# Optimization experiments

Hardware: AMD Instinct MI355X
Metric: run time of the kernel (lower is better)

## Reference

```python
import jax, jax.numpy as jnp
import numpy as np
import math

D_MODEL = 1024
NUM_HEADS = 16
D_HEAD = D_MODEL // NUM_HEADS  # 64
B, S = 2, 1024


def setup_inputs() -> dict:
    key = jax.random.key(0)
    ks = jax.random.split(key, 11)
    s = 1.0 / math.sqrt(D_MODEL)
    inp = {
        "Q": jax.random.normal(ks[0], (B, S, D_MODEL), jnp.float32),
        "K": jax.random.normal(ks[1], (B, S, D_MODEL), jnp.float32),
        "V": jax.random.normal(ks[2], (B, S, D_MODEL), jnp.float32),
        "Wq": jax.random.normal(ks[3], (D_MODEL, D_MODEL), jnp.float32) * s,
        "bq": jnp.zeros((D_MODEL,), jnp.float32),
        "Wk": jax.random.normal(ks[4], (D_MODEL, D_MODEL), jnp.float32) * s,
        "bk": jnp.zeros((D_MODEL,), jnp.float32),
        "Wv": jax.random.normal(ks[5], (D_MODEL, D_MODEL), jnp.float32) * s,
        "bv": jnp.zeros((D_MODEL,), jnp.float32),
        "Wo": jax.random.normal(ks[6], (D_MODEL, D_MODEL), jnp.float32) * s,
        "bo": jnp.zeros((D_MODEL,), jnp.float32),
    }
    return inp


def _linear(x, W, b):
    # torch nn.Linear: x @ W.T + b
    return jnp.einsum("bsd,ed->bse", x, W) + b


def _split_heads(x):
    # Faithful to original: view(b, s, d_head, num_heads).transpose(1, 2)
    # -> 'heads' axis has size d_head, per-head dim is num_heads.
    b, s, _ = x.shape
    return x.reshape(b, s, D_HEAD, NUM_HEADS).transpose(0, 2, 1, 3)  # [b, d_head, s, num_heads]


def reference(Q, K, V, Wq, bq, Wk, bk, Wv, bv, Wo, bo):
    q = _split_heads(_linear(Q, Wq, bq))  # [b, h=d_head, s, e=num_heads]
    k = _split_heads(_linear(K, Wk, bk))
    v = _split_heads(_linear(V, Wv, bv))
    scale = 1.0 / math.sqrt(D_MODEL)  # original scales by sqrt(d_model)
    scores = jnp.einsum("bhqe,bhke->bhqk", q, k) * scale
    attn = jax.nn.softmax(scores, axis=-1)
    ctx = jnp.einsum("bhqk,bhke->bhqe", attn, v)  # [b, d_head, s, num_heads]
    # combine_heads: transpose(1,2) then flatten last two dims
    b, h, s, e = ctx.shape
    merged = ctx.transpose(0, 2, 1, 3).reshape(b, s, h * e)
    return _linear(merged, Wo, bo)
```

## Files before the change

kernel.cpp:

```cpp
#include <hip/hip_runtime.h>
#include <cstdint>
#include <cstddef>
#include <math.h>

typedef _Float16 f16;
typedef _Float16 f16x8 __attribute__((ext_vector_type(8)));
typedef _Float16 f16x4 __attribute__((ext_vector_type(4)));
typedef float f32x4 __attribute__((ext_vector_type(4)));
typedef float f32x16 __attribute__((ext_vector_type(16)));

#define MFMA16(A, B, C) __builtin_amdgcn_mfma_f32_16x16x32_f16((A), (B), (C), 0, 0, 0)
#define MFMA32(A, B, C) __builtin_amdgcn_mfma_f32_32x32x16_f16((A), (B), (C), 0, 0, 0)

#if __has_builtin(__builtin_amdgcn_exp2f)
#define EXP2(x) __builtin_amdgcn_exp2f(x)
#else
#define EXP2(x) exp2f(x)
#endif

__device__ __forceinline__ f16x8 ld8(const f16* p) { return *(const f16x8*)p; }
__device__ __forceinline__ void st8(f16* p, f16x8 v) { *(f16x8*)p = v; }
__device__ __forceinline__ void st4(f16* p, f16x4 v) { *(f16x4*)p = v; }

__device__ __forceinline__ void gll16(const f16* g, f16* l) {
    __builtin_amdgcn_global_load_lds(
        (__attribute__((address_space(1))) void*)(uintptr_t)g,
        (__attribute__((address_space(3))) void*)(unsigned)(uintptr_t)l,
        16, 0, 0);
}

__global__ __launch_bounds__(256) void cast_all(
    const float* __restrict__ Q, const float* __restrict__ K, const float* __restrict__ V,
    const float* __restrict__ Wq, const float* __restrict__ Wk, const float* __restrict__ Wv,
    const float* __restrict__ Wo, f16* __restrict__ dst)
{
    size_t e = ((size_t)blockIdx.x * 256 + threadIdx.x) * 8;
    const float* s; size_t r;
    if (e < 2097152)      { s = Q;  r = e; }
    else if (e < 4194304) { s = K;  r = e - 2097152; }
    else if (e < 6291456) { s = V;  r = e - 4194304; }
    else if (e < 7340032) { s = Wq; r = e - 6291456; }
    else if (e < 8388608) { s = Wk; r = e - 7340032; }
    else if (e < 9437184) { s = Wv; r = e - 8388608; }
    else                  { s = Wo; r = e - 9437184; }
    float4 a = *(const float4*)(s + r);
    float4 b = *(const float4*)(s + r + 4);
    f16x8 o;
    o[0]=(f16)a.x; o[1]=(f16)a.y; o[2]=(f16)a.z; o[3]=(f16)a.w;
    o[4]=(f16)b.x; o[5]=(f16)b.y; o[6]=(f16)b.z; o[7]=(f16)b.w;
    st8(dst + e, o);
}

__global__ __launch_bounds__(256) void qkv_gemm(
    const f16* __restrict__ ws, const float* __restrict__ bq,
    const float* __restrict__ bk, const float* __restrict__ bv,
    f16* __restrict__ outbase)
{
    const int bx = blockIdx.x, bm = blockIdx.y;
    const int mat = bx >> 3, bn = bx & 7;
    const f16* A  = ws + (size_t)mat * 2097152;
    const f16* Bw = ws + 6291456 + (size_t)mat * 1048576;
    const float* bias = (mat == 0) ? bq : (mat == 1) ? bk : bv;
    f16* C = outbase + (size_t)mat * 2097152;

    __shared__ f16 As[2 * 4096];
    __shared__ f16 Bs[2 * 8192];
    const int t = threadIdx.x;
    const int w = t >> 6, lane = t & 63, l5 = lane & 31, hh = lane >> 5;
    const int swz = ((lane & 7) ^ (lane >> 3)) * 8;
    const int l7 = l5 & 7;

    const f16* Ap = A  + (size_t)(bm * 64  + w * 8 + (lane >> 3)) * 1024 + swz;
    const f16* Bp = Bw + (size_t)(bn * 128 + w * 8 + (lane >> 3)) * 1024 + swz;

    f32x16 acc[2] = {};

    gll16(Ap,         &As[w * 512]);
    gll16(Ap + 32768, &As[2048 + w * 512]);
    #pragma unroll
    for (int q = 0; q < 4; ++q)
        gll16(Bp + q * 32768, &Bs[q * 2048 + w * 512]);

    #pragma unroll 2
    for (int kt = 0; kt < 16; ++kt) {
        const int cur = kt & 1;
        __syncthreads();
        if (kt < 15) {
            const f16* Ak = Ap + (kt + 1) * 64;
            const f16* Bk = Bp + (kt + 1) * 64;
            f16* Ad = &As[(cur ^ 1) * 4096 + w * 512];
            f16* Bd = &Bs[(cur ^ 1) * 8192 + w * 512];
            gll16(Ak,         Ad);
            gll16(Ak + 32768, Ad + 2048);
            #pragma unroll
            for (int q = 0; q < 4; ++q)
                gll16(Bk + q * 32768, Bd + q * 2048);
        }
        const f16* Ac = &As[cur * 4096];
        const f16* Bc = &Bs[cur * 8192];
        #pragma unroll
        for (int ks = 0; ks < 4; ++ks) {
            const int c = ks * 2 + hh;
            f16x8 bfr = ld8(&Bc[(w * 32 + l5) * 64 + ((c ^ l7) * 8)]);
            f16x8 af0 = ld8(&Ac[ l5       * 64 + ((c ^ l7) * 8)]);
            f16x8 af1 = ld8(&Ac[(32 + l5) * 64 + ((c ^ l7) * 8)]);
            acc[0] = MFMA32(af0, bfr, acc[0]);
            acc[1] = MFMA32(af1, bfr, acc[1]);
        }
    }

    const float qscale = 0.04508422002778009f;
    const int n = bn * 128 + w * 32 + l5;
    const float bv_ = bias[n];
    if (mat == 0) {
        #pragma unroll
        for (int i = 0; i < 2; ++i)
            #pragma unroll
            for (int r = 0; r < 16; ++r) {
                const int m = bm * 64 + i * 32 + (r & 3) + 8 * (r >> 2) + 4 * hh;
                C[(size_t)m * 1024 + n] = (f16)((acc[i][r] + bv_) * qscale);
            }
    } else if (mat == 1) {
        #pragma unroll
        for (int i = 0; i < 2; ++i)
            #pragma unroll
            for (int r = 0; r < 16; ++r) {
                const int m = bm * 64 + i * 32 + (r & 3) + 8 * (r >> 2) + 4 * hh;
                C[(size_t)m * 1024 + n] = (f16)(acc[i][r] + bv_);
            }
    } else {
        const int hN = n >> 4, eN = n & 15;
        #pragma unroll
        for (int i = 0; i < 2; ++i)
            #pragma unroll
            for (int g = 0; g < 4; ++g) {
                const int m0 = bm * 64 + i * 32 + 8 * g + 4 * hh;
                const int bb = m0 >> 10, s0 = m0 & 1023;
                f16x4 pv;
                pv[0] = (f16)(acc[i][4 * g + 0] + bv_);
                pv[1] = (f16)(acc[i][4 * g + 1] + bv_);
                pv[2] = (f16)(acc[i][4 * g + 2] + bv_);
                pv[3] = (f16)(acc[i][4 * g + 3] + bv_);
                st4(C + ((size_t)((bb * 64 + hN) * 16 + eN)) * 1024 + s0, pv);
            }
    }
}

__global__ __launch_bounds__(256, 4) void attn(
    const f16* __restrict__ qlin, const f16* __restrict__ klin,
    const f16* __restrict__ vT, f16* __restrict__ merged)
{
    __shared__ f16 Ks[2][2048];
    __shared__ f16 Vs[2][2176];
    __shared__ f16 Ps[4][1280];

    const int t = threadIdx.x;
    const int w = t >> 6, lane = t & 63;
    const int l5 = lane & 31, hh = lane >> 5, lg = (lane >> 4) & 3, ll = lane & 15;
    const int h = blockIdx.x, qt = blockIdx.y, b = blockIdx.z;

    const int rowQ0 = b * 1024 + qt * 128;
    const int colh = h * 16;

    f16x8 qf = ld8(qlin + (size_t)(rowQ0 + w * 32 + l5) * 1024 + colh + hh * 8);

    const int sp = ((lane & 7) - (lane >> 3)) & 7;
    const f16* kptr = klin + (size_t)(b * 1024 + w * 32 + (lane >> 3) * 4 + (sp >> 1)) * 1024
                      + colh + (sp & 1) * 8;
    const int ve = t >> 4, vk = (t & 15) * 8;
    const f16* vptr = vT + (size_t)((b * 64 + h) * 16 + ve) * 1024 + vk;
    f16* vdst0 = &Vs[0][ve * 136 + vk];
    f16* vdst1 = &Vs[1][ve * 136 + vk];

    int offKa[4];
    #pragma unroll
    for (int mt = 0; mt < 4; ++mt) {
        const int r = mt * 32 + l5, g = r >> 2;
        offKa[mt] = g * 64 + (((((r & 3) * 2 + hh) + g) & 7) * 8);
    }

    float lsum = 0.f;
    f32x4 O0 = {}, O1 = {};
    f16* Pw = Ps[w];

    f16x8 vv = ld8(vptr);
    gll16(kptr, &Ks[0][w * 512]);
    st8(vdst0, vv);

    for (int kt = 0; kt < 8; ++kt) {
        const int cur = kt & 1;
        if (kt < 7) vv = ld8(vptr + (kt + 1) * 128);
        __syncthreads();
        if (kt < 7) {
            gll16(kptr + (size_t)(kt + 1) * 131072, &Ks[cur ^ 1][w * 512]);
            st8(cur ? vdst0 : vdst1, vv);
        }

        #pragma unroll
        for (int mt = 0; mt < 4; ++mt) {
            f16x8 ka = ld8(&Ks[cur][offKa[mt]]);
            f32x16 Sz = {};
            f32x16 S = MFMA32(ka, qf, Sz);

            #pragma unroll
            for (int g = 0; g < 4; ++g) {
                float p0 = EXP2(S[4 * g + 0]);
                float p1 = EXP2(S[4 * g + 1]);
                float p2 = EXP2(S[4 * g + 2]);
                float p3 = EXP2(S[4 * g + 3]);
                lsum += (p0 + p1) + (p2 + p3);
                f16x4 pk;
                pk[0] = (f16)p0; pk[1] = (f16)p1; pk[2] = (f16)p2; pk[3] = (f16)p3;
                st4(&Pw[l5 * 40 + g * 8 + hh * 4], pk);
            }

            f16x8 va  = ld8(&Vs[cur][ll * 136 + mt * 32 + lg * 8]);
            f16x8 pb0 = ld8(&Pw[ll * 40 + lg * 8]);
            f16x8 pb1 = ld8(&Pw[(16 + ll) * 40 + lg * 8]);
            O0 = MFMA16(va, pb0, O0);
            O1 = MFMA16(va, pb1, O1);
        }
    }

    lsum += __shfl_xor(lsum, 32);
    const float i0 = 1.f / __shfl(lsum, ll);
    const float i1 = 1.f / __shfl(lsum, 16 + ll);

    f16x4 o0, o1;
    o0[0]=(f16)(O0[0]*i0); o0[1]=(f16)(O0[1]*i0); o0[2]=(f16)(O0[2]*i0); o0[3]=(f16)(O0[3]*i0);
    o1[0]=(f16)(O1[0]*i1); o1[1]=(f16)(O1[1]*i1); o1[2]=(f16)(O1[2]*i1); o1[3]=(f16)(O1[3]*i1);
    const size_t q0 = rowQ0 + w * 32 + ll;
    st4(merged + q0 * 1024 + colh + lg * 4, o0);
    st4(merged + (q0 + 16) * 1024 + colh + lg * 4, o1);
}

__global__ __launch_bounds__(256) void o_gemm(
    const f16* __restrict__ A, const f16* __restrict__ Bw,
    const float* __restrict__ bias, float* __restrict__ Cf)
{
    const int bn = blockIdx.x, bm = blockIdx.y;
    __shared__ f16 As[2 * 4096];
    __shared__ f16 Bs[2 * 4096];
    const int t = threadIdx.x;
    const int w = t >> 6, lane = t & 63, l5 = lane & 31, hh = lane >> 5;
    const int wr = w >> 1, wc = w & 1;
    const int swz = ((lane & 7) ^ (lane >> 3)) * 8;
    const int l7 = l5 & 7;

    const f16* Ap = A  + (size_t)(bm * 64 + w * 8 + (lane >> 3)) * 1024 + swz;
    const f16* Bp = Bw + (size_t)(bn * 64 + w * 8 + (lane >> 3)) * 1024 + swz;

    f32x16 acc = {};

    gll16(Ap,         &As[w * 512]);
    gll16(Ap + 32768, &As[2048 + w * 512]);
    gll16(Bp,         &Bs[w * 512]);
    gll16(Bp + 32768, &Bs[2048 + w * 512]);

    #pragma unroll 2
    for (int kt = 0; kt < 16; ++kt) {
        const int cur = kt & 1;
        __syncthreads();
        if (kt < 15) {
            const f16* Ak = Ap + (kt + 1) * 64;
            const f16* Bk = Bp + (kt + 1) * 64;
            f16* Ad = &As[(cur ^ 1) * 4096 + w * 512];
            f16* Bd = &Bs[(cur ^ 1) * 4096 + w * 512];
            gll16(Ak,         Ad);
            gll16(Ak + 32768, Ad + 2048);
            gll16(Bk,         Bd);
            gll16(Bk + 32768, Bd + 2048);
        }
        const f16* Ac = &As[cur * 4096];
        const f16* Bc = &Bs[cur * 4096];
        #pragma unroll
        for (int ks = 0; ks < 4; ++ks) {
            const int c = ks * 2 + hh;
            f16x8 af = ld8(&Ac[(wr * 32 + l5) * 64 + ((c ^ l7) * 8)]);
            f16x8 bf = ld8(&Bc[(wc * 32 + l5) * 64 + ((c ^ l7) * 8)]);
            acc = MFMA32(af, bf, acc);
        }
    }

    const int n = bn * 64 + wc * 32 + l5;
    const float bv_ = bias[n];
    #pragma unroll
    for (int r = 0; r < 16; ++r) {
        const int m = bm * 64 + wr * 32 + (r & 3) + 8 * (r >> 2) + 4 * hh;
        Cf[(size_t)m * 1024 + n] = acc[r] + bv_;
    }
}

extern "C" void kernel_launch(void* const* d_in, const int* in_sizes, int n_in,
                              void* d_out, int out_size, void* d_ws, size_t ws_size,
                              hipStream_t stream) {
    (void)in_sizes; (void)n_in; (void)out_size; (void)ws_size;
    const float* Q  = (const float*)d_in[0];
    const float* K  = (const float*)d_in[1];
    const float* V  = (const float*)d_in[2];
    const float* Wq = (const float*)d_in[3];
    const float* bq = (const float*)d_in[4];
    const float* Wk = (const float*)d_in[5];
    const float* bk = (const float*)d_in[6];
    const float* Wv = (const float*)d_in[7];
    const float* bv = (const float*)d_in[8];
    const float* Wo = (const float*)d_in[9];
    const float* bo = (const float*)d_in[10];
    float* out = (float*)d_out;

    f16* ws = (f16*)d_ws;
    f16* qlin   = ws + 10485760;
    f16* klin   = ws + 12582912;
    f16* vT     = ws + 14680064;
    f16* merged = ws + 16777216;
    f16* Woc    = ws + 9437184;

    cast_all<<<5120, 256, 0, stream>>>(Q, K, V, Wq, Wk, Wv, Wo, ws);
    qkv_gemm<<<dim3(24, 32), 256, 0, stream>>>(ws, bq, bk, bv, qlin);
    attn<<<dim3(64, 8, 2), 256, 0, stream>>>(qlin, klin, vT, merged);
    o_gemm<<<dim3(16, 32), 256, 0, stream>>>(merged, Woc, bo, out);
}
```

Before: 160.2 us.

## Enlarge QKV GEMM block tile to 128x128 with 2x2 warp grid

```diff
diff --git a/kernel.cpp b/kernel.cpp
--- a/kernel.cpp
+++ b/kernel.cpp
@@ -51,7 +51,7 @@
     st8(dst + e, o);
 }
 
-__global__ __launch_bounds__(256) void qkv_gemm(
+__global__ __launch_bounds__(256, 2) void qkv_gemm(
     const f16* __restrict__ ws, const float* __restrict__ bq,
     const float* __restrict__ bk, const float* __restrict__ bv,
     f16* __restrict__ outbase)
@@ -63,86 +63,90 @@
     const float* bias = (mat == 0) ? bq : (mat == 1) ? bk : bv;
     f16* C = outbase + (size_t)mat * 2097152;
 
-    __shared__ f16 As[2 * 4096];
-    __shared__ f16 Bs[2 * 8192];
+    __shared__ f16 As[2][8192];
+    __shared__ f16 Bs[2][8192];
     const int t = threadIdx.x;
     const int w = t >> 6, lane = t & 63, l5 = lane & 31, hh = lane >> 5;
+    const int wr = w >> 1, wc = w & 1;
     const int swz = ((lane & 7) ^ (lane >> 3)) * 8;
     const int l7 = l5 & 7;
 
-    const f16* Ap = A  + (size_t)(bm * 64  + w * 8 + (lane >> 3)) * 1024 + swz;
-    const f16* Bp = Bw + (size_t)(bn * 128 + w * 8 + (lane >> 3)) * 1024 + swz;
-
-    f32x16 acc[2] = {};
-
-    gll16(Ap,         &As[w * 512]);
-    gll16(Ap + 32768, &As[2048 + w * 512]);
+    const f16* Ap = A  + (size_t)(bm * 128 + w * 32 + (lane >> 3)) * 1024 + swz;
+    const f16* Bp = Bw + (size_t)(bn * 128 + w * 32 + (lane >> 3)) * 1024 + swz;
+
+    f32x16 acc[2][2] = {};
+
     #pragma unroll
-    for (int q = 0; q < 4; ++q)
-        gll16(Bp + q * 32768, &Bs[q * 2048 + w * 512]);
-
-    #pragma unroll 2
+    for (int q = 0; q < 4; ++q) {
+        gll16(Ap + q * 8192, &As[0][(w * 32 + q * 8) * 64]);
+        gll16(Bp + q * 8192, &Bs[0][(w * 32 + q * 8) * 64]);
+    }
+
     for (int kt = 0; kt < 16; ++kt) {
         const int cur = kt & 1;
         __syncthreads();
         if (kt < 15) {
             const f16* Ak = Ap + (kt + 1) * 64;
             const f16* Bk = Bp + (kt + 1) * 64;
-            f16* Ad = &As[(cur ^ 1) * 4096 + w * 512];
-            f16* Bd = &Bs[(cur ^ 1) * 8192 + w * 512];
-            gll16(Ak,         Ad);
-            gll16(Ak + 32768, Ad + 2048);
-            #pragma unroll
-            for (int q = 0; q < 4; ++q)
-                gll16(Bk + q * 32768, Bd + q * 2048);
-        }
-        const f16* Ac = &As[cur * 4096];
-        const f16* Bc = &Bs[cur * 8192];
+            #pragma unroll
+            for (int q = 0; q < 4; ++q) {
+                gll16(Ak + q * 8192, &As[cur ^ 1][(w * 32 + q * 8) * 64]);
+                gll16(Bk + q * 8192, &Bs[cur ^ 1][(w * 32 + q * 8) * 64]);
+            }
+        }
+        const f16* Ac = As[cur];
+        const f16* Bc = Bs[cur];
         #pragma unroll
         for (int ks = 0; ks < 4; ++ks) {
-            const int c = ks * 2 + hh;
-            f16x8 bfr = ld8(&Bc[(w * 32 + l5) * 64 + ((c ^ l7) * 8)]);
-            f16x8 af0 = ld8(&Ac[ l5       * 64 + ((c ^ l7) * 8)]);
-            f16x8 af1 = ld8(&Ac[(32 + l5) * 64 + ((c ^ l7) * 8)]);
-            acc[0] = MFMA32(af0, bfr, acc[0]);
-            acc[1] = MFMA32(af1, bfr, acc[1]);
+            const int c = ((ks * 2 + hh) ^ l7) * 8;
+            f16x8 af0 = ld8(&Ac[(wr * 64      + l5) * 64 + c]);
+            f16x8 af1 = ld8(&Ac[(wr * 64 + 32 + l5) * 64 + c]);
+            f16x8 bf0 = ld8(&Bc[(wc * 64      + l5) * 64 + c]);
+            f16x8 bf1 = ld8(&Bc[(wc * 64 + 32 + l5) * 64 + c]);
+            acc[0][0] = MFMA32(af0, bf0, acc[0][0]);
+            acc[0][1] = MFMA32(af0, bf1, acc[0][1]);
+            acc[1][0] = MFMA32(af1, bf0, acc[1][0]);
+            acc[1][1] = MFMA32(af1, bf1, acc[1][1]);
         }
     }
 
     const float qscale = 0.04508422002778009f;
-    const int n = bn * 128 + w * 32 + l5;
-    const float bv_ = bias[n];
-    if (mat == 0) {
-        #pragma unroll
-        for (int i = 0; i < 2; ++i)
-            #pragma unroll
-            for (int r = 0; r < 16; ++r) {
-                const int m = bm * 64 + i * 32 + (r & 3) + 8 * (r >> 2) + 4 * hh;
-                C[(size_t)m * 1024 + n] = (f16)((acc[i][r] + bv_) * qscale);
-            }
-    } else if (mat == 1) {
-        #pragma unroll
-        for (int i = 0; i < 2; ++i)
-            #pragma unroll
-            for (int r = 0; r < 16; ++r) {
-                const int m = bm * 64 + i * 32 + (r & 3) + 8 * (r >> 2) + 4 * hh;
-                C[(size_t)m * 1024 + n] = (f16)(acc[i][r] + bv_);
-            }
-    } else {
-        const int hN = n >> 4, eN = n & 15;
-        #pragma unroll
-        for (int i = 0; i < 2; ++i)
-            #pragma unroll
-            for (int g = 0; g < 4; ++g) {
-                const int m0 = bm * 64 + i * 32 + 8 * g + 4 * hh;
-                const int bb = m0 >> 10, s0 = m0 & 1023;
-                f16x4 pv;
-                pv[0] = (f16)(acc[i][4 * g + 0] + bv_);
-                pv[1] = (f16)(acc[i][4 * g + 1] + bv_);
-                pv[2] = (f16)(acc[i][4 * g + 2] + bv_);
-                pv[3] = (f16)(acc[i][4 * g + 3] + bv_);
-                st4(C + ((size_t)((bb * 64 + hN) * 16 + eN)) * 1024 + s0, pv);
-            }
+    #pragma unroll
+    for (int j = 0; j < 2; ++j) {
+        const int n = bn * 128 + wc * 64 + j * 32 + l5;
+        const float bv_ = bias[n];
+        if (mat == 0) {
+            #pragma unroll
+            for (int i = 0; i < 2; ++i)
+                #pragma unroll
+                for (int r = 0; r < 16; ++r) {
+                    const int m = bm * 128 + wr * 64 + i * 32 + (r & 3) + 8 * (r >> 2) + 4 * hh;
+                    C[(size_t)m * 1024 + n] = (f16)((acc[i][j][r] + bv_) * qscale);
+                }
+        } else if (mat == 1) {
+            #pragma unroll
+            for (int i = 0; i < 2; ++i)
+                #pragma unroll
+                for (int r = 0; r < 16; ++r) {
+                    const int m = bm * 128 + wr * 64 + i * 32 + (r & 3) + 8 * (r >> 2) + 4 * hh;
+                    C[(size_t)m * 1024 + n] = (f16)(acc[i][j][r] + bv_);
+                }
+        } else {
+            const int hN = n >> 4, eN = n & 15;
+            #pragma unroll
+            for (int i = 0; i < 2; ++i)
+                #pragma unroll
+                for (int g = 0; g < 4; ++g) {
+                    const int m0 = bm * 128 + wr * 64 + i * 32 + 8 * g + 4 * hh;
+                    const int bb = m0 >> 10, s0 = m0 & 1023;
+                    f16x4 pv;
+                    pv[0] = (f16)(acc[i][j][4 * g + 0] + bv_);
+                    pv[1] = (f16)(acc[i][j][4 * g + 1] + bv_);
+                    pv[2] = (f16)(acc[i][j][4 * g + 2] + bv_);
+                    pv[3] = (f16)(acc[i][j][4 * g + 3] + bv_);
+                    st4(C + ((size_t)((bb * 64 + hN) * 16 + eN)) * 1024 + s0, pv);
+                }
+        }
     }
 }
 
@@ -316,7 +320,7 @@
     f16* Woc    = ws + 9437184;
 
     cast_all<<<5120, 256, 0, stream>>>(Q, K, V, Wq, Wk, Wv, Wo, ws);
-    qkv_gemm<<<dim3(24, 32), 256, 0, stream>>>(ws, bq, bk, bv, qlin);
+    qkv_gemm<<<dim3(24, 16), 256, 0, stream>>>(ws, bq, bk, bv, qlin);
     attn<<<dim3(64, 8, 2), 256, 0, stream>>>(qlin, klin, vT, merged);
     o_gemm<<<dim3(16, 32), 256, 0, stream>>>(merged, Woc, bo, out);
 }
```

Result: no change. 161.4 us (+0.7%).
